# Kernel optimization log

Hardware: AMD Instinct MI355X
Metric: run time of the kernel (lower is better)

## Reference

```python
import jax, jax.numpy as jnp
import numpy as np

NUM_HEADS = 4
NUM_GROUPS = 8
EPS = 1e-5


def setup_inputs() -> dict:
    key = jax.random.key(0)
    ks = jax.random.split(key, 4)
    B, C, H, W = 16, 512, 64, 64
    x = jax.random.normal(ks[0], (B, C, H, W), dtype=jnp.float32)
    norm_g = jnp.ones((C,), dtype=jnp.float32)
    norm_b = jnp.zeros((C,), dtype=jnp.float32)
    qkv_w = jax.random.normal(ks[1], (3 * C, C), dtype=jnp.float32) * (1.0 / np.sqrt(C))
    qkv_b = jnp.zeros((3 * C,), dtype=jnp.float32)
    proj_w = jax.random.normal(ks[2], (C, C), dtype=jnp.float32) * (1.0 / np.sqrt(C))
    proj_b = jnp.zeros((C,), dtype=jnp.float32)
    return {"x": x, "norm_g": norm_g, "norm_b": norm_b,
            "qkv_w": qkv_w, "qkv_b": qkv_b, "proj_w": proj_w, "proj_b": proj_b}


def _group_norm(x, g, b):
    B, C, H, W = x.shape
    xg = x.reshape(B, NUM_GROUPS, C // NUM_GROUPS, H, W)
    mean = xg.mean(axis=(2, 3, 4), keepdims=True)
    var = xg.var(axis=(2, 3, 4), keepdims=True)
    xn = ((xg - mean) * jax.lax.rsqrt(var + EPS)).reshape(B, C, H, W)
    return xn * g[None, :, None, None] + b[None, :, None, None]


def reference(x, norm_g, norm_b, qkv_w, qkv_b, proj_w, proj_b):
    B, C, H, W = x.shape
    d = C // NUM_HEADS
    scale = d ** (-0.5)
    xn = _group_norm(x, norm_g, norm_b)
    # 1x1 conv == channel GEMM
    qkv = jnp.einsum('oc,bchw->bohw', qkv_w, xn) + qkv_b[None, :, None, None]
    qkv = qkv.reshape(B, NUM_HEADS, 3 * d, H * W)
    q, k, v = qkv[:, :, :d], qkv[:, :, d:2 * d], qkv[:, :, 2 * d:]
    # Faithful to the original (degenerate) einsum: q's last axis is summed out
    attn = jnp.einsum('bnhq,bnhk->bnhk', q, k) * scale
    attn = jax.nn.softmax(attn, axis=-1)
    out = jnp.einsum('bnhk,bnhv->bnhv', attn, v)
    out = out.reshape(B, C, H, W)
    out = jnp.einsum('oc,bchw->bohw', proj_w, out) + proj_b[None, :, None, None]
    return out + x
```

## Files before the change

kernel.cpp:

```cpp
#include <hip/hip_runtime.h>

#define CC 512
#define SS 4096
#define GELEMS 262144

typedef __attribute__((ext_vector_type(8))) __bf16 bf16x8;
typedef __attribute__((ext_vector_type(4))) float f32x4;
typedef __attribute__((ext_vector_type(4))) unsigned short us4;
typedef __attribute__((ext_vector_type(8))) unsigned short us8;

__device__ __forceinline__ unsigned short f2bf(float f) {
  unsigned int u = __float_as_uint(f);
  u += 0x7fffu + ((u >> 16) & 1u);
  return (unsigned short)(u >> 16);
}
__device__ __forceinline__ int qrow(int cv) { return ((cv >> 7) * 384) + 256 + (cv & 127); }

__device__ __forceinline__ void gl_lds16(const void* g, void* l) {
  __builtin_amdgcn_global_load_lds((const __attribute__((address_space(1))) unsigned int*)g,
                                   (__attribute__((address_space(3))) unsigned int*)l, 16, 0, 0);
}

__global__ __launch_bounds__(256) void k_front(const float* __restrict__ x,
    const float* __restrict__ pw, const float* __restrict__ qw,
    float* __restrict__ part, float* __restrict__ mw) {
  __shared__ float red[8];
  __shared__ __align__(16) unsigned short Asb[64 * 32];
  __shared__ __align__(16) unsigned short Bsb[64 * 32];
  int t = threadIdx.x;
  int w = t >> 6, l = t & 63;
  if (blockIdx.x < 1024) {
    int bid = blockIdx.x;
    int bg = bid >> 3, sp = bid & 7;
    const float4* p = (const float4*)(x + (size_t)bg * GELEMS + (size_t)sp * 32768);
    float s = 0.f, ss = 0.f;
#pragma unroll
    for (int i = 0; i < 32; ++i) {
      float4 v = p[i * 256 + t];
      s += v.x + v.y + v.z + v.w;
      ss += v.x * v.x + v.y * v.y + v.z * v.z + v.w * v.w;
    }
#pragma unroll
    for (int off = 32; off; off >>= 1) { s += __shfl_down(s, off); ss += __shfl_down(ss, off); }
    if (l == 0) { red[w * 2] = s; red[w * 2 + 1] = ss; }
    __syncthreads();
    if (t == 0) {
      part[bid * 2] = red[0] + red[2] + red[4] + red[6];
      part[bid * 2 + 1] = red[1] + red[3] + red[5] + red[7];
    }
  } else {
    int bb = blockIdx.x - 1024;
    int bm = (bb >> 3) * 64;
    int bn = (bb & 7) * 64;
    int wm = (w >> 1) * 32, wn = (w & 1) * 32;
    int fr = l & 15, fk = (l >> 4) * 8;
    f32x4 acc[2][2] = {};
    for (int k0 = 0; k0 < 512; k0 += 32) {
#pragma unroll
      for (int i = 0; i < 2; ++i) {
        int e = i * 256 + t;
        int row = e >> 3, f4 = e & 7;
        float4 v = *(const float4*)&pw[(size_t)(bm + row) * 512 + k0 + f4 * 4];
        us4 pk; pk[0] = f2bf(v.x); pk[1] = f2bf(v.y); pk[2] = f2bf(v.z); pk[3] = f2bf(v.w);
        *(us4*)&Asb[row * 32 + f4 * 4] = pk;
      }
#pragma unroll
      for (int i = 0; i < 2; ++i) {
        int e = i * 256 + t;
        int row = e >> 4, f4 = e & 15;
        float4 v = *(const float4*)&qw[(size_t)qrow(k0 + row) * 512 + bn + f4 * 4];
        Bsb[(f4 * 4 + 0) * 32 + row] = f2bf(v.x);
        Bsb[(f4 * 4 + 1) * 32 + row] = f2bf(v.y);
        Bsb[(f4 * 4 + 2) * 32 + row] = f2bf(v.z);
        Bsb[(f4 * 4 + 3) * 32 + row] = f2bf(v.w);
      }
      __syncthreads();
      bf16x8 a[2], bfr[2];
#pragma unroll
      for (int i = 0; i < 2; ++i) a[i] = *(const bf16x8*)&Asb[(wm + i * 16 + fr) * 32 + fk];
#pragma unroll
      for (int j = 0; j < 2; ++j) bfr[j] = *(const bf16x8*)&Bsb[(wn + j * 16 + fr) * 32 + fk];
#pragma unroll
      for (int i = 0; i < 2; ++i)
#pragma unroll
        for (int j = 0; j < 2; ++j)
          acc[i][j] = __builtin_amdgcn_mfma_f32_16x16x32_bf16(a[i], bfr[j], acc[i][j], 0, 0, 0);
      __syncthreads();
    }
#pragma unroll
    for (int i = 0; i < 2; ++i)
#pragma unroll
      for (int j = 0; j < 2; ++j)
#pragma unroll
        for (int r = 0; r < 4; ++r) {
          int row = bm + wm + i * 16 + (l >> 4) * 4 + r;
          int col = bn + wn + j * 16 + (l & 15);
          mw[(size_t)row * 512 + col] = acc[i][j][r];
        }
  }
}

__global__ __launch_bounds__(256) void k_prep(const float* __restrict__ part,
    const float* __restrict__ ng, const float* __restrict__ nb,
    const float* __restrict__ mw, const float* __restrict__ pw,
    const float* __restrict__ qb, const float* __restrict__ pb,
    unsigned short* __restrict__ mwa, float* __restrict__ bias2) {
  int t = threadIdx.x;
  __shared__ float S1[512], S2[512];
  __shared__ float ms[8], rs[8];
  int b = (blockIdx.x < 2048) ? (blockIdx.x >> 7) : ((blockIdx.x - 2048) >> 3);
  {
    int g = t >> 5, i = t & 31;
    const float* p = part + ((size_t)(b * 8 + g)) * 16;
    float S = 0.f, Q = 0.f;
    if (i < 8) { S = p[i * 2]; Q = p[i * 2 + 1]; }
#pragma unroll
    for (int off = 16; off; off >>= 1) { S += __shfl_down(S, off, 32); Q += __shfl_down(Q, off, 32); }
    if (i == 0) {
      float mean = S * (1.f / 262144.f);
      float var = Q * (1.f / 262144.f) - mean * mean;
      ms[g] = mean; rs[g] = rsqrtf(var + 1e-5f);
    }
  }
  __syncthreads();
  if (blockIdx.x < 2048) {
    int r4 = (blockIdx.x & 127) * 4;
#pragma unroll
    for (int q = 0; q < 2; ++q) { int c = t + q * 256; S1[c] = rs[c >> 6] * ng[c]; }
    __syncthreads();
    int c2 = r4 + (t >> 6), c = (t & 63) * 8;
    const float4* mr = (const float4*)&mw[(size_t)c2 * 512 + c];
    float4 m0 = mr[0], m1 = mr[1];
    const float4* ar = (const float4*)&S1[c];
    float4 a0 = ar[0], a1 = ar[1];
    float v[8] = {m0.x*a0.x, m0.y*a0.y, m0.z*a0.z, m0.w*a0.w,
                  m1.x*a1.x, m1.y*a1.y, m1.z*a1.z, m1.w*a1.w};
    if (c2 >= c && c2 < c + 8) v[c2 - c] += 1.0f;
    us8 o;
#pragma unroll
    for (int j = 0; j < 8; ++j) o[j] = f2bf(v[j]);
    int wblk = c2 >> 6, i2 = (c2 >> 4) & 3, fr = c2 & 15;
    int step = c >> 5, fq = (c >> 3) & 3;
    size_t addr = ((((size_t)(b * 8 + wblk) * 4 + i2) * 16 + step) * 64 + (fq * 16 + fr)) * 8;
    *(us8*)&mwa[addr] = o;
  } else {
    int c2b = ((blockIdx.x - 2048) & 7) * 64;
    int w = t >> 6, l = t & 63;
#pragma unroll
    for (int q = 0; q < 2; ++q) {
      int c = t + q * 256;
      float A = rs[c >> 6] * ng[c];
      S1[c] = nb[c] - ms[c >> 6] * A;
      S2[c] = qb[qrow(c)];
    }
    __syncthreads();
    for (int it = 0; it < 16; ++it) {
      int c2 = c2b + w * 16 + it;
      const float4* pwr = (const float4*)&pw[(size_t)c2 * 512];
      const float4* mwr = (const float4*)&mw[(size_t)c2 * 512];
      float4 p0 = pwr[l * 2], p1 = pwr[l * 2 + 1];
      float4 m0 = mwr[l * 2], m1 = mwr[l * 2 + 1];
      const float4* qs = (const float4*)&S2[l * 8];
      const float4* bs = (const float4*)&S1[l * 8];
      float4 q0 = qs[0], q1 = qs[1], b0 = bs[0], b1 = bs[1];
      float acc = p0.x * q0.x + p0.y * q0.y + p0.z * q0.z + p0.w * q0.w
                + p1.x * q1.x + p1.y * q1.y + p1.z * q1.z + p1.w * q1.w
                + m0.x * b0.x + m0.y * b0.y + m0.z * b0.z + m0.w * b0.w
                + m1.x * b1.x + m1.y * b1.y + m1.z * b1.z + m1.w * b1.w;
#pragma unroll
      for (int off = 32; off; off >>= 1) acc += __shfl_down(acc, off);
      if (l == 0) bias2[b * 512 + c2] = acc + pb[c2];
    }
  }
}

__global__ __launch_bounds__(512, 4) void k_fused6(const unsigned short* __restrict__ mwa,
    const float* __restrict__ x, const float* __restrict__ bias2,
    float* __restrict__ out) {
  __shared__ __align__(16) unsigned short Bt[32768];
  int bid0 = blockIdx.x;
  int bid = 1023 - ((bid0 & 7) * 128 + (bid0 >> 3));
  int b = bid >> 6, st = bid & 63;
  int s0 = st * 64;
  int t = threadIdx.x, w = t >> 6, l = t & 63;
  int m0 = w * 64;
  int fr = l & 15, fq = l >> 4;
  const unsigned short* Ag = mwa + ((size_t)(b * 8 + w)) * 32768;

  const float* xb = x + ((size_t)b * 512) * SS + s0 + l;
  float cur[8];
#pragma unroll
  for (int j = 0; j < 8; ++j) cur[j] = xb[(size_t)(w * 8 + j) * SS];
#pragma unroll
  for (int i = 0; i < 8; ++i) {
    float nxt[8];
    if (i < 7) {
#pragma unroll
      for (int j = 0; j < 8; ++j) nxt[j] = xb[(size_t)(((i + 1) * 8 + w) * 8 + j) * SS];
    }
    int g = i * 8 + w;
    int kc = g >> 4, s8l = (g >> 2) & 3, fql = g & 3;
    us8 o;
#pragma unroll
    for (int j = 0; j < 8; ++j) o[j] = f2bf(cur[j]);
    *(us8*)&Bt[kc * 8192 + (s8l * 4 + (l >> 4)) * 512 + (fql * 16 + (l & 15)) * 8] = o;
#pragma unroll
    for (int j = 0; j < 8; ++j) cur[j] = nxt[j];
  }
  bf16x8 fa[2][4];
#pragma unroll
  for (int i = 0; i < 4; ++i)
    fa[0][i] = *(const bf16x8*)&Ag[(i * 16 + 0) * 512 + l * 8];
  __syncthreads();

  f32x4 acc[4][4] = {};
#pragma unroll
  for (int step = 0; step < 16; ++step) {
    const int cur2 = step & 1;
    if (step < 15) {
#pragma unroll
      for (int i = 0; i < 4; ++i)
        fa[cur2 ^ 1][i] = *(const bf16x8*)&Ag[(i * 16 + step + 1) * 512 + l * 8];
    }
    bf16x8 fb[4];
#pragma unroll
    for (int j = 0; j < 4; ++j)
      fb[j] = *(const bf16x8*)&Bt[(step >> 2) * 8192 + ((step & 3) * 4 + j) * 512 + l * 8];
#pragma unroll
    for (int i = 0; i < 4; ++i)
#pragma unroll
      for (int j = 0; j < 4; ++j)
        acc[i][j] = __builtin_amdgcn_mfma_f32_16x16x32_bf16(fa[cur2][i], fb[j], acc[i][j], 0, 0, 0);
  }

  float4 bi[4];
#pragma unroll
  for (int i = 0; i < 4; ++i)
    bi[i] = *(const float4*)&bias2[b * 512 + m0 + i * 16 + fq * 4];
  __syncthreads();
  float* Ls = (float*)Bt;
  float* ob = out + (size_t)b * 512 * SS + s0;
#pragma unroll
  for (int i = 0; i < 4; ++i) {
    float bir[4] = {bi[i].x, bi[i].y, bi[i].z, bi[i].w};
#pragma unroll
    for (int j = 0; j < 4; ++j)
#pragma unroll
      for (int r = 0; r < 4; ++r)
        Ls[w * 1024 + (fq * 4 + r) * 64 + (((j ^ fq) & 3) * 16 + fr)] = acc[i][j][r] + bir[r];
    asm volatile("s_waitcnt lgkmcnt(0)" ::: "memory");
    __builtin_amdgcn_sched_barrier(0);
#pragma unroll
    for (int q = 0; q < 4; ++q) {
      int row16 = q * 4 + (l >> 4);
      int colR = (l & 15) * 4;
      f32x4 v = *(const f32x4*)&Ls[w * 1024 + row16 * 64 + (colR ^ (q * 16))];
      __builtin_nontemporal_store(v, (f32x4*)&ob[(size_t)(m0 + i * 16 + row16) * SS + colR]);
    }
    asm volatile("s_waitcnt lgkmcnt(0)" ::: "memory");
  }
}

__global__ __launch_bounds__(256) void k_stats(const float* __restrict__ x, float* __restrict__ part) {
  int bid = blockIdx.x;
  int bg = bid >> 3, sp = bid & 7;
  const float4* p = (const float4*)(x + (size_t)bg * GELEMS + (size_t)sp * 32768);
  int t = threadIdx.x;
  float s = 0.f, ss = 0.f;
#pragma unroll
  for (int i = 0; i < 32; ++i) {
    float4 v = p[i * 256 + t];
    s += v.x + v.y + v.z + v.w;
    ss += v.x * v.x + v.y * v.y + v.z * v.z + v.w * v.w;
  }
#pragma unroll
  for (int off = 32; off; off >>= 1) { s += __shfl_down(s, off); ss += __shfl_down(ss, off); }
  __shared__ float red[8];
  int wid = t >> 6;
  if ((t & 63) == 0) { red[wid * 2] = s; red[wid * 2 + 1] = ss; }
  __syncthreads();
  if (t == 0) {
    part[bid * 2] = red[0] + red[2] + red[4] + red[6];
    part[bid * 2 + 1] = red[1] + red[3] + red[5] + red[7];
  }
}

__global__ __launch_bounds__(256) void k_mw(const float* __restrict__ pw, const float* __restrict__ qw,
                                            float* __restrict__ mw, unsigned short* __restrict__ mwbf) {
  __shared__ __align__(16) unsigned short Asb[64 * 32];
  __shared__ __align__(16) unsigned short Bsb[64 * 32];
  int t = threadIdx.x;
  int bm = (blockIdx.x >> 3) * 64;
  int bn = (blockIdx.x & 7) * 64;
  int w = t >> 6, l = t & 63;
  int wm = (w >> 1) * 32, wn = (w & 1) * 32;
  int fr = l & 15, fk = (l >> 4) * 8;
  f32x4 acc[2][2] = {};
  for (int k0 = 0; k0 < 512; k0 += 32) {
#pragma unroll
    for (int i = 0; i < 2; ++i) {
      int e = i * 256 + t;
      int row = e >> 3, f4 = e & 7;
      float4 v = *(const float4*)&pw[(size_t)(bm + row) * 512 + k0 + f4 * 4];
      us4 pk; pk[0] = f2bf(v.x); pk[1] = f2bf(v.y); pk[2] = f2bf(v.z); pk[3] = f2bf(v.w);
      *(us4*)&Asb[row * 32 + f4 * 4] = pk;
    }
#pragma unroll
    for (int i = 0; i < 2; ++i) {
      int e = i * 256 + t;
      int row = e >> 4, f4 = e & 15;
      float4 v = *(const float4*)&qw[(size_t)qrow(k0 + row) * 512 + bn + f4 * 4];
      Bsb[(f4 * 4 + 0) * 32 + row] = f2bf(v.x);
      Bsb[(f4 * 4 + 1) * 32 + row] = f2bf(v.y);
      Bsb[(f4 * 4 + 2) * 32 + row] = f2bf(v.z);
      Bsb[(f4 * 4 + 3) * 32 + row] = f2bf(v.w);
    }
    __syncthreads();
    bf16x8 a[2], bfr[2];
#pragma unroll
    for (int i = 0; i < 2; ++i) a[i] = *(const bf16x8*)&Asb[(wm + i * 16 + fr) * 32 + fk];
#pragma unroll
    for (int j = 0; j < 2; ++j) bfr[j] = *(const bf16x8*)&Bsb[(wn + j * 16 + fr) * 32 + fk];
#pragma unroll
    for (int i = 0; i < 2; ++i)
#pragma unroll
      for (int j = 0; j < 2; ++j)
        acc[i][j] = __builtin_amdgcn_mfma_f32_16x16x32_bf16(a[i], bfr[j], acc[i][j], 0, 0, 0);
    __syncthreads();
  }
#pragma unroll
  for (int i = 0; i < 2; ++i)
#pragma unroll
    for (int j = 0; j < 2; ++j)
#pragma unroll
      for (int r = 0; r < 4; ++r) {
        int row = bm + wm + i * 16 + (l >> 4) * 4 + r;
        int col = bn + wn + j * 16 + (l & 15);
        float v = acc[i][j][r];
        mw[(size_t)row * 512 + col] = v;
        mwbf[(size_t)row * 512 + col] = f2bf(v);
      }
}

__global__ __launch_bounds__(256) void k_fin(const float* __restrict__ part,
    const float* __restrict__ ng, const float* __restrict__ nb,
    float* __restrict__ afac, float* __restrict__ bcv, int np) {
  int b = blockIdx.x, t = threadIdx.x;
  __shared__ float mean_s[8], rstd_s[8];
  int g = t >> 5, i = t & 31;
  float S = 0.f, Q = 0.f;
  for (int k = i; k < np; k += 32) {
    S += part[((b * 8 + g) * np + k) * 2];
    Q += part[((b * 8 + g) * np + k) * 2 + 1];
  }
#pragma unroll
  for (int off = 16; off; off >>= 1) { S += __shfl_down(S, off, 32); Q += __shfl_down(Q, off, 32); }
  if (i == 0) {
    float mean = S * (1.f / 262144.f);
    float var = Q * (1.f / 262144.f) - mean * mean;
    mean_s[g] = mean;
    rstd_s[g] = rsqrtf(var + 1e-5f);
  }
  __syncthreads();
#pragma unroll
  for (int q = 0; q < 2; ++q) {
    int c = t + q * 256;
    int gg = c >> 6;
    float A = rstd_s[gg] * ng[c];
    afac[b * 512 + c] = A;
    bcv[b * 512 + c] = nb[c] - mean_s[gg] * A;
  }
}

__global__ __launch_bounds__(256) void k_bias2(const float* __restrict__ mw,
    const float* __restrict__ bcv, const float* __restrict__ pw,
    const float* __restrict__ qb, const float* __restrict__ pb, float* __restrict__ bias2) {
  int b = blockIdx.x >> 3, c2b = (blockIdx.x & 7) * 64;
  int t = threadIdx.x, w = t >> 6, l = t & 63;
  __shared__ float Bcs[512], Qbs[512];
  for (int i = t; i < 512; i += 256) { Bcs[i] = bcv[b * 512 + i]; Qbs[i] = qb[qrow(i)]; }
  __syncthreads();
  for (int it = 0; it < 16; ++it) {
    int c2 = c2b + w * 16 + it;
    const float4* pwr = (const float4*)&pw[(size_t)c2 * 512];
    const float4* mwr = (const float4*)&mw[(size_t)c2 * 512];
    float4 p0 = pwr[l * 2], p1 = pwr[l * 2 + 1];
    float4 m0 = mwr[l * 2], m1 = mwr[l * 2 + 1];
    const float4* qs = (const float4*)&Qbs[l * 8];
    const float4* bs = (const float4*)&Bcs[l * 8];
    float4 q0 = qs[0], q1 = qs[1], b0 = bs[0], b1 = bs[1];
    float acc = p0.x * q0.x + p0.y * q0.y + p0.z * q0.z + p0.w * q0.w
              + p1.x * q1.x + p1.y * q1.y + p1.z * q1.z + p1.w * q1.w
              + m0.x * b0.x + m0.y * b0.y + m0.z * b0.z + m0.w * b0.w
              + m1.x * b1.x + m1.y * b1.y + m1.z * b1.z + m1.w * b1.w;
#pragma unroll
    for (int off = 32; off; off >>= 1) acc += __shfl_down(acc, off);
    if (l == 0) bias2[b * 512 + c2] = acc + pb[c2];
  }
}

__global__ __launch_bounds__(256) void k_gemm_fb(const unsigned short* __restrict__ mwbf,
    const float* __restrict__ x, const float* __restrict__ afac,
    const float* __restrict__ bias2, float* __restrict__ out) {
  __shared__ __align__(16) unsigned short Ab[128 * 32];
  __shared__ __align__(16) unsigned short Bb[128 * 32];
  __shared__ float Afs[512];
  int bid0 = blockIdx.x;
  int bid = (bid0 & 7) * 256 + (bid0 >> 3);
  int b = bid >> 7, rem = bid & 127, nt = rem >> 2, mt = rem & 3;
  int m0 = mt * 128, s0 = nt * 128;
  int t = threadIdx.x, w = t >> 6, l = t & 63;
  int wm = (w >> 1) * 64, wn = (w & 1) * 64;
  const unsigned short* Ag = mwbf + (size_t)m0 * CC;
  int lr = l >> 2, lk = (l & 3) * 8;
  int fr = l & 15, fk = (l >> 4) * 8;
  for (int i = t; i < 512; i += 256) Afs[i] = afac[b * CC + i];
  __syncthreads();
  f32x4 acc[4][4] = {};
  for (int k0 = 0; k0 < CC; k0 += 32) {
#pragma unroll
    for (int q = 0; q < 2; ++q) {
      int row = w * 32 + q * 16;
      gl_lds16(Ag + (size_t)(row + lr) * CC + k0 + lk, &Ab[row * 32]);
    }
#pragma unroll
    for (int i2 = 0; i2 < 4; ++i2) {
      int e = i2 * 256 + t;
      int row = e >> 5, f4 = e & 31;
      float4 v = *(const float4*)&x[((size_t)(b * CC + k0 + row)) * SS + s0 + f4 * 4];
      float a = Afs[k0 + row];
      Bb[(f4 * 4 + 0) * 32 + row] = f2bf(v.x * a);
      Bb[(f4 * 4 + 1) * 32 + row] = f2bf(v.y * a);
      Bb[(f4 * 4 + 2) * 32 + row] = f2bf(v.z * a);
      Bb[(f4 * 4 + 3) * 32 + row] = f2bf(v.w * a);
    }
    __syncthreads();
    bf16x8 af[4], bfr[4];
#pragma unroll
    for (int i = 0; i < 4; ++i) af[i] = *(const bf16x8*)&Ab[(wm + i * 16 + fr) * 32 + fk];
#pragma unroll
    for (int j = 0; j < 4; ++j) bfr[j] = *(const bf16x8*)&Bb[(wn + j * 16 + fr) * 32 + fk];
#pragma unroll
    for (int i = 0; i < 4; ++i)
#pragma unroll
      for (int j = 0; j < 4; ++j)
        acc[i][j] = __builtin_amdgcn_mfma_f32_16x16x32_bf16(af[i], bfr[j], acc[i][j], 0, 0, 0);
    __syncthreads();
  }
  int c2b = m0 + wm, sb = s0 + wn;
  float bi[4][4];
#pragma unroll
  for (int i = 0; i < 4; ++i)
#pragma unroll
    for (int r = 0; r < 4; ++r)
      bi[i][r] = bias2[b * CC + c2b + i * 16 + (l >> 4) * 4 + r];
#pragma unroll
  for (int i = 0; i < 4; ++i)
#pragma unroll
    for (int j = 0; j < 4; ++j)
#pragma unroll
      for (int r = 0; r < 4; ++r) {
        int c2 = c2b + i * 16 + (l >> 4) * 4 + r;
        int s = sb + j * 16 + (l & 15);
        size_t oi = ((size_t)(b * CC + c2)) * SS + s;
        out[oi] = acc[i][j][r] + bi[i][r] + x[oi];
      }
}

extern "C" void kernel_launch(void* const* d_in, const int* in_sizes, int n_in,
                              void* d_out, int out_size, void* d_ws, size_t ws_size,
                              hipStream_t stream) {
  const float* x = (const float*)d_in[0];
  const float* ng = (const float*)d_in[1];
  const float* nb = (const float*)d_in[2];
  const float* qw = (const float*)d_in[3];
  const float* qb = (const float*)d_in[4];
  const float* pw = (const float*)d_in[5];
  const float* pb = (const float*)d_in[6];
  float* out = (float*)d_out;
  char* ws = (char*)d_ws;

  float* part = (float*)(ws + 0);
  float* afac = (float*)(ws + 65536);
  float* bcv = (float*)(ws + 98304);
  float* bias2 = (float*)(ws + 131072);
  float* mw = (float*)(ws + 163840);
  unsigned short* mwbf = (unsigned short*)(ws + 1212416);
  unsigned short* mwa = (unsigned short*)(ws + 1736704);

  bool fast = ws_size >= 10125312ull;

  if (fast) {
    k_front<<<1088, 256, 0, stream>>>(x, pw, qw, part, mw);
    k_prep<<<2176, 256, 0, stream>>>(part, ng, nb, mw, pw, qb, pb, mwa, bias2);
    k_fused6<<<1024, 512, 0, stream>>>(mwa, x, bias2, out);
  } else {
    k_stats<<<1024, 256, 0, stream>>>(x, part);
    k_mw<<<64, 256, 0, stream>>>(pw, qw, mw, mwbf);
    k_fin<<<16, 256, 0, stream>>>(part, ng, nb, afac, bcv, 8);
    k_bias2<<<128, 256, 0, stream>>>(mw, bcv, pw, qb, pb, bias2);
    k_gemm_fb<<<2048, 256, 0, stream>>>(mwbf, x, afac, bias2, out);
  }
}
```

Before: 120.1 us.

## Emit bf16 copy of x in stats pass and read it in fused GEMM

The statistics pass now also writes a bf16 copy of x to workspace. The fused GEMM reads that copy with 16-byte vector loads and transposes it in registers, instead of issuing strided scalar fp32 loads and converting them. The LDS B-tile layout gains an XOR swizzle to reduce bank conflicts on the MFMA operand reads. Total DRAM traffic stays about the same, since an extra 64 MB write offsets the halved read in the GEMM. The fast path now needs a much larger workspace; if that is not available, the slower fallback path runs.

```diff
diff --git a/kernel.cpp b/kernel.cpp
--- a/kernel.cpp
+++ b/kernel.cpp
@@ -21,9 +21,9 @@
                                    (__attribute__((address_space(3))) unsigned int*)l, 16, 0, 0);
 }
 
-__global__ __launch_bounds__(256) void k_front(const float* __restrict__ x,
+__global__ __launch_bounds__(256) void k_front2(const float* __restrict__ x,
     const float* __restrict__ pw, const float* __restrict__ qw,
-    float* __restrict__ part, float* __restrict__ mw) {
+    unsigned short* __restrict__ xbf, float* __restrict__ part, float* __restrict__ mw) {
   __shared__ float red[8];
   __shared__ __align__(16) unsigned short Asb[64 * 32];
   __shared__ __align__(16) unsigned short Bsb[64 * 32];
@@ -33,12 +33,15 @@
     int bid = blockIdx.x;
     int bg = bid >> 3, sp = bid & 7;
     const float4* p = (const float4*)(x + (size_t)bg * GELEMS + (size_t)sp * 32768);
+    unsigned short* ob = xbf + (size_t)bg * GELEMS + (size_t)sp * 32768;
     float s = 0.f, ss = 0.f;
 #pragma unroll
     for (int i = 0; i < 32; ++i) {
       float4 v = p[i * 256 + t];
       s += v.x + v.y + v.z + v.w;
       ss += v.x * v.x + v.y * v.y + v.z * v.z + v.w * v.w;
+      us4 o; o[0] = f2bf(v.x); o[1] = f2bf(v.y); o[2] = f2bf(v.z); o[3] = f2bf(v.w);
+      *(us4*)&ob[(i * 256 + t) * 4] = o;
     }
 #pragma unroll
     for (int off = 32; off; off >>= 1) { s += __shfl_down(s, off); ss += __shfl_down(ss, off); }
@@ -174,8 +177,8 @@
   }
 }
 
-__global__ __launch_bounds__(512, 4) void k_fused6(const unsigned short* __restrict__ mwa,
-    const float* __restrict__ x, const float* __restrict__ bias2,
+__global__ __launch_bounds__(512, 4) void k_fused10(const unsigned short* __restrict__ mwa,
+    const unsigned short* __restrict__ xbf, const float* __restrict__ bias2,
     float* __restrict__ out) {
   __shared__ __align__(16) unsigned short Bt[32768];
   int bid0 = blockIdx.x;
@@ -187,25 +190,41 @@
   int fr = l & 15, fq = l >> 4;
   const unsigned short* Ag = mwa + ((size_t)(b * 8 + w)) * 32768;
 
-  const float* xb = x + ((size_t)b * 512) * SS + s0 + l;
-  float cur[8];
-#pragma unroll
-  for (int j = 0; j < 8; ++j) cur[j] = xb[(size_t)(w * 8 + j) * SS];
-#pragma unroll
-  for (int i = 0; i < 8; ++i) {
-    float nxt[8];
-    if (i < 7) {
-#pragma unroll
-      for (int j = 0; j < 8; ++j) nxt[j] = xb[(size_t)(((i + 1) * 8 + w) * 8 + j) * SS];
-    }
-    int g = i * 8 + w;
+  {
+    int g = w * 8 + (l >> 3), sw = l & 7;
+    const unsigned short* src = xbf + ((size_t)(b * 512 + g * 8)) * SS + s0 + sw * 8;
+    uint4 r[8];
+#pragma unroll
+    for (int p = 0; p < 8; ++p) r[p] = *(const uint4*)(src + (size_t)p * SS);
     int kc = g >> 4, s8l = (g >> 2) & 3, fql = g & 3;
-    us8 o;
-#pragma unroll
-    for (int j = 0; j < 8; ++j) o[j] = f2bf(cur[j]);
-    *(us8*)&Bt[kc * 8192 + (s8l * 4 + (l >> 4)) * 512 + (fql * 16 + (l & 15)) * 8] = o;
-#pragma unroll
-    for (int j = 0; j < 8; ++j) cur[j] = nxt[j];
+#pragma unroll
+    for (int j = 0; j < 8; ++j) {
+      uint4 ov;
+      {
+        unsigned int a0 = (j & 4) ? ((j & 2) ? r[0].w : r[0].z) : ((j & 2) ? r[0].y : r[0].x);
+        unsigned int b0 = (j & 4) ? ((j & 2) ? r[1].w : r[1].z) : ((j & 2) ? r[1].y : r[1].x);
+        unsigned int a1 = (j & 4) ? ((j & 2) ? r[2].w : r[2].z) : ((j & 2) ? r[2].y : r[2].x);
+        unsigned int b1 = (j & 4) ? ((j & 2) ? r[3].w : r[3].z) : ((j & 2) ? r[3].y : r[3].x);
+        unsigned int a2 = (j & 4) ? ((j & 2) ? r[4].w : r[4].z) : ((j & 2) ? r[4].y : r[4].x);
+        unsigned int b2 = (j & 4) ? ((j & 2) ? r[5].w : r[5].z) : ((j & 2) ? r[5].y : r[5].x);
+        unsigned int a3 = (j & 4) ? ((j & 2) ? r[6].w : r[6].z) : ((j & 2) ? r[6].y : r[6].x);
+        unsigned int b3 = (j & 4) ? ((j & 2) ? r[7].w : r[7].z) : ((j & 2) ? r[7].y : r[7].x);
+        if (j & 1) {
+          ov.x = (b0 & 0xffff0000u) | (a0 >> 16);
+          ov.y = (b1 & 0xffff0000u) | (a1 >> 16);
+          ov.z = (b2 & 0xffff0000u) | (a2 >> 16);
+          ov.w = (b3 & 0xffff0000u) | (a3 >> 16);
+        } else {
+          ov.x = (b0 << 16) | (a0 & 0xffffu);
+          ov.y = (b1 << 16) | (a1 & 0xffffu);
+          ov.z = (b2 << 16) | (a2 & 0xffffu);
+          ov.w = (b3 << 16) | (a3 & 0xffffu);
+        }
+      }
+      int s = sw * 8 + j;
+      int jj = s >> 4, frr = (s & 15) ^ (fql << 1);
+      *(uint4*)&Bt[kc * 8192 + (s8l * 4 + jj) * 512 + (fql * 16 + frr) * 8] = ov;
+    }
   }
   bf16x8 fa[2][4];
 #pragma unroll
@@ -213,6 +232,7 @@
     fa[0][i] = *(const bf16x8*)&Ag[(i * 16 + 0) * 512 + l * 8];
   __syncthreads();
 
+  int lslot = (fq * 16 + (fr ^ (fq << 1))) * 8;
   f32x4 acc[4][4] = {};
 #pragma unroll
   for (int step = 0; step < 16; ++step) {
@@ -225,7 +245,7 @@
     bf16x8 fb[4];
 #pragma unroll
     for (int j = 0; j < 4; ++j)
-      fb[j] = *(const bf16x8*)&Bt[(step >> 2) * 8192 + ((step & 3) * 4 + j) * 512 + l * 8];
+      fb[j] = *(const bf16x8*)&Bt[(step >> 2) * 8192 + ((step & 3) * 4 + j) * 512 + lslot];
 #pragma unroll
     for (int i = 0; i < 4; ++i)
 #pragma unroll
@@ -487,13 +507,14 @@
   float* mw = (float*)(ws + 163840);
   unsigned short* mwbf = (unsigned short*)(ws + 1212416);
   unsigned short* mwa = (unsigned short*)(ws + 1736704);
-
-  bool fast = ws_size >= 10125312ull;
+  unsigned short* xbf = (unsigned short*)(ws + 10125312);
+
+  bool fast = ws_size >= 77234176ull;
 
   if (fast) {
-    k_front<<<1088, 256, 0, stream>>>(x, pw, qw, part, mw);
+    k_front2<<<1088, 256, 0, stream>>>(x, pw, qw, xbf, part, mw);
     k_prep<<<2176, 256, 0, stream>>>(part, ng, nb, mw, pw, qb, pb, mwa, bias2);
-    k_fused6<<<1024, 512, 0, stream>>>(mwa, x, bias2, out);
+    k_fused10<<<1024, 512, 0, stream>>>(mwa, xbf, bias2, out);
   } else {
     k_stats<<<1024, 256, 0, stream>>>(x, part);
     k_mw<<<64, 256, 0, stream>>>(pw, qw, mw, mwbf);
```

New measurement: 122.6 us. 2.0% more time.
